# Performance work log

Hardware: AMD Instinct MI355X
Metric: run time of the kernel (lower is better)

The kernel has to match this reference:

```python
import jax, jax.numpy as jnp
import numpy as np

B, L, N = 32, 512, 512          # batch, seq_len, enc_in (num variables = token dim)
D, H, EL, DF = 512, 8, 2, 2048  # d_model, n_heads (hardcoded 8 in FourierBlock), e_layers, d_ff
PRED, K, MODES = 96, 25, 64     # pred_len, moving_avg kernel, fourier modes (low select)
E = D // H


def setup_inputs() -> dict:
    key = jax.random.key(0)
    ks = jax.random.split(key, 16)
    s = 0.02
    return {
        "x_enc": jax.random.normal(ks[0], (B, L, N), jnp.float32),
        "x_mark_enc": jax.random.normal(ks[1], (B, L, 4), jnp.float32),
        "x_dec": jax.random.normal(ks[2], (B, 144, N), jnp.float32),
        "x_mark_dec": jax.random.normal(ks[3], (B, 144, 4), jnp.float32),
        "W_trend": jax.random.normal(ks[4], (L, PRED), jnp.float32) * s,
        "b_trend": jnp.zeros((PRED,), jnp.float32),
        "W_emb": jax.random.normal(ks[5], (L, D), jnp.float32) * s,
        "b_emb": jnp.zeros((D,), jnp.float32),
        "Wq": jax.random.normal(ks[6], (EL, D, D), jnp.float32) * s,
        "bq": jnp.zeros((EL, D), jnp.float32),
        "Wk": jax.random.normal(ks[7], (EL, D, D), jnp.float32) * s,
        "bk": jnp.zeros((EL, D), jnp.float32),
        "Wv": jax.random.normal(ks[8], (EL, D, D), jnp.float32) * s,
        "bv": jnp.zeros((EL, D), jnp.float32),
        "fw_r": jax.random.uniform(ks[9], (EL, H, E, E, MODES), jnp.float32) / (D * D),
        "fw_i": jax.random.uniform(ks[10], (EL, H, E, E, MODES), jnp.float32) / (D * D),
        "Wo": jax.random.normal(ks[11], (EL, D, D), jnp.float32) * s,
        "bo": jnp.zeros((EL, D), jnp.float32),
        "W1": jax.random.normal(ks[12], (EL, DF, D), jnp.float32) * s,
        "W2": jax.random.normal(ks[13], (EL, D, DF), jnp.float32) * s,
        "ln_g": jnp.ones((D,), jnp.float32),
        "ln_b": jnp.zeros((D,), jnp.float32),
        "W_head": jax.random.normal(ks[14], (D, PRED), jnp.float32) * s,
        "b_head": jnp.zeros((PRED,), jnp.float32),
    }


def series_decomp(x, k):
    # moving average over axis=1 with edge replication padding (Autoformer style)
    pad = (k - 1) // 2
    xp = jnp.concatenate([jnp.repeat(x[:, :1], pad, axis=1), x,
                          jnp.repeat(x[:, -1:], pad, axis=1)], axis=1)
    c = jnp.cumsum(xp, axis=1)
    c = jnp.concatenate([jnp.zeros_like(c[:, :1]), c], axis=1)
    mean = (c[:, k:] - c[:, :-k]) / k
    return x - mean, mean


def fourier_attn(x, Wq, bq, Wk, bk, Wv, bv, fw, Wo, bo):
    # AutoCorrelationLayer wrapping FourierBlock (k/v projections computed but unused)
    b, n, d = x.shape
    q = (x @ Wq + bq).reshape(b, n, H, E)
    _k = (x @ Wk + bk).reshape(b, n, H, E)
    _v = (x @ Wv + bv).reshape(b, n, H, E)
    xq = jnp.transpose(q, (0, 2, 3, 1))        # [B,H,E,N]
    x_ft = jnp.fft.rfft(xq, axis=-1)           # [B,H,E,N//2+1]
    m = fw.shape[-1]
    # low-frequency mode select: index = range(m); out_ft[..., wi] = einsum('bhi,hio->bho')
    out_sel = jnp.einsum('bhim,hiom->bhom', x_ft[..., :m], fw)
    out_ft = jnp.zeros((b, H, E, n // 2 + 1), x_ft.dtype).at[..., :m].set(out_sel)
    xt = jnp.fft.irfft(out_ft, n=n, axis=-1)   # [B,H,E,N]
    out = xt.reshape(b, n, H * E)              # replicates torch .view(B, L, -1) on [B,H,E,L]
    return out @ Wo + bo


def encoder_layer(x, Wq, bq, Wk, bk, Wv, bv, fw, Wo, bo, W1, W2):
    x = x + fourier_attn(x, Wq, bq, Wk, bk, Wv, bv, fw, Wo, bo)
    x, _ = series_decomp(x, K)
    y = jax.nn.gelu(x @ W1.T, approximate=False) @ W2.T  # 1x1 convs, bias=False
    x, _ = series_decomp(x + y, K)
    return x


def my_layernorm(x, g, b):
    mu = jnp.mean(x, -1, keepdims=True)
    var = jnp.var(x, -1, keepdims=True)
    xh = (x - mu) / jnp.sqrt(var + 1e-5) * g + b
    return xh - jnp.mean(xh, axis=1, keepdims=True)  # my_Layernorm: subtract seq-mean


def reference(x_enc, x_mark_enc, x_dec, x_mark_dec, W_trend, b_trend, W_emb, b_emb,
              Wq, bq, Wk, bk, Wv, bv, fw_r, fw_i, Wo, bo, W1, W2, ln_g, ln_b,
              W_head, b_head):
    seasonal, trend = series_decomp(x_enc, K)                         # [B,L,N]
    trend_out = jnp.einsum('bln,lp->bpn', trend, W_trend) + b_trend[None, :, None]
    enc = jnp.einsum('bln,ld->bnd', seasonal, W_emb) + b_emb          # variate tokens [B,N,D]
    for i in range(EL):
        fw = fw_r[i] + 1j * fw_i[i]
        enc = encoder_layer(enc, Wq[i], bq[i], Wk[i], bk[i], Wv[i], bv[i],
                            fw, Wo[i], bo[i], W1[i], W2[i])
    enc = my_layernorm(enc, ln_g, ln_b)
    seasonal_out = jnp.transpose(enc @ W_head + b_head, (0, 2, 1))    # [B,pred,N]
    return seasonal_out + trend_out
```

## Files before the change

kernel.cpp:

```cpp
#include <hip/hip_runtime.h>
#include <math.h>


typedef unsigned short ushort_t;
typedef unsigned int uint_t;
using bf16x8_t = __attribute__((ext_vector_type(8))) short;
using f32x4_t  = __attribute__((ext_vector_type(4))) float;
using u16x8_t  = __attribute__((ext_vector_type(8))) unsigned short;

__device__ __forceinline__ unsigned short f2b(float x) {
    union { float f; uint_t u; } c; c.f = x;
    uint_t r = c.u + 0x7fffu + ((c.u >> 16) & 1u);
    return (unsigned short)(r >> 16);
}
__device__ __forceinline__ float b2f(unsigned short h) {
    union { uint_t u; float f; } c; c.u = ((uint_t)h) << 16; return c.f;
}
__device__ __forceinline__ float gelu_exact(float v) {
    return 0.5f * v * (1.0f + erff(v * 0.70710678118654752f));
}

#define GCAST(p) ((const __attribute__((address_space(1))) void*)(p))
#define LCAST(p) ((__attribute__((address_space(3))) void*)(p))

enum { ME_F32 = 0, ME_BF16, ME_DCBIAS_BF16, ME_BIASCOL_BF16,
       ME_BIASCOL_ACCB16, ME_GELU_BF16, ME_RESB_BF16, ME_TREND };

template<int EPI>
__global__ __launch_bounds__(512)
void mgemm_k(const ushort_t* __restrict__ A, const ushort_t* __restrict__ B,
             const float* __restrict__ bias, const ushort_t* __restrict__ Resb,
             void* __restrict__ Cv,
             int M, int N, int K, int ldc, int ldres,
             long sA, long sB, long sC, long sRes)
{
    const int gx = gridDim.x, gy = gridDim.y;
    const int nwg = gx * gy * gridDim.z;
    const int lin = (blockIdx.z * gy + blockIdx.y) * gx + blockIdx.x;
    const int cpx = nwg >> 3;
    const int swz = (nwg & 7) ? lin : ((lin & 7) * cpx + (lin >> 3));
    const int bx = swz % gx;
    const int t2 = swz / gx;
    const int by = t2 % gy;
    const int bz = t2 / gy;

    A += bz * sA;
    B += bz * sB;
    const int m0 = by * 128, n0 = bx * 128;

    __shared__ __align__(16) ushort_t As[3][4096];
    __shared__ __align__(16) ushort_t Bs[3][4096];

    const int tid = threadIdx.x;
    const int wave = tid >> 6, lane = tid & 63;
    const int wr = wave >> 1, wc = wave & 1;

    f32x4_t acc[2][4] = {};

    const int srow = tid >> 2;
    const int skof = (tid & 3) * 8;

    const ushort_t* ga = A + (long)(m0 + srow) * K + skof;
    const ushort_t* gb = B + (long)(n0 + srow) * K + skof;
    const int nt = K >> 5;

#define STG(s, bidx) { const long ko = (long)(s) << 5; \
    __builtin_amdgcn_global_load_lds(GCAST(ga + ko), LCAST(As[bidx] + wave * 512), 16, 0, 0); \
    __builtin_amdgcn_global_load_lds(GCAST(gb + ko), LCAST(Bs[bidx] + wave * 512), 16, 0, 0); }

    STG(0, 0)
    STG(1, 1)

    const int kg = (lane >> 4) * 8;
    int cb = 0;

    for (int t = 0; t < nt; ++t) {
        if (t + 1 < nt) { asm volatile("s_waitcnt vmcnt(2)" ::: "memory"); }
        else            { asm volatile("s_waitcnt vmcnt(0)" ::: "memory"); }
        __builtin_amdgcn_s_barrier();
        asm volatile("" ::: "memory");
        __builtin_amdgcn_sched_barrier(0);
        if (t + 2 < nt) { int nb = cb + 2; if (nb >= 3) nb -= 3; STG(t + 2, nb) }

        bf16x8_t a[2], b[4];
        #pragma unroll
        for (int i = 0; i < 2; ++i)
            a[i] = *(const bf16x8_t*)&As[cb][(wr * 32 + i * 16 + (lane & 15)) * 32 + kg];
        #pragma unroll
        for (int j = 0; j < 4; ++j)
            b[j] = *(const bf16x8_t*)&Bs[cb][(wc * 64 + j * 16 + (lane & 15)) * 32 + kg];
        #pragma unroll
        for (int i = 0; i < 2; ++i)
            #pragma unroll
            for (int j = 0; j < 4; ++j)
                acc[i][j] = __builtin_amdgcn_mfma_f32_16x16x32_bf16(a[i], b[j], acc[i][j], 0, 0, 0);
        ++cb; if (cb >= 3) cb = 0;
    }
#undef STG

    float*    Cf  = (float*)Cv + bz * sC;
    ushort_t* Cb  = (ushort_t*)Cv + bz * sC;
    const ushort_t* R = Resb ? Resb + bz * sRes : nullptr;

    #pragma unroll
    for (int i = 0; i < 2; ++i) {
        #pragma unroll
        for (int j = 0; j < 4; ++j) {
            #pragma unroll
            for (int r = 0; r < 4; ++r) {
                int gm = m0 + wr * 32 + i * 16 + (lane >> 4) * 4 + r;
                int gn = n0 + wc * 64 + j * 16 + (lane & 15);
                float v = acc[i][j][r];
                long idx = (long)gm * ldc + gn;
                if (EPI == ME_F32)               Cf[idx] = v;
                else if (EPI == ME_BF16)         Cb[idx] = f2b(v);
                else if (EPI == ME_DCBIAS_BF16)  Cb[idx] = f2b(v + (gn == 0 ? 512.f * bias[gm] : 0.f));
                else if (EPI == ME_BIASCOL_BF16) Cb[idx] = f2b(v + bias[gn]);
                else if (EPI == ME_BIASCOL_ACCB16) Cb[idx] = f2b(b2f(Cb[idx]) + v + bias[gn]);
                else if (EPI == ME_GELU_BF16)    Cb[idx] = f2b(gelu_exact(v));
                else if (EPI == ME_RESB_BF16)    Cb[idx] = f2b(v + b2f(R[(long)gm * ldres + gn]));
                else if (EPI == ME_TREND) { if (gm < 96) Cf[idx] = v + bias[gm]; }
            }
        }
    }
}

__global__ __launch_bounds__(256)
void fmix_k(const ushort_t* __restrict__ A2, const ushort_t* __restrict__ B2,
            ushort_t* __restrict__ OS)
{
    const int hm = blockIdx.x;
    const int h = hm >> 6, m = hm & 63;
    __shared__ __align__(16) ushort_t As[32 * 128];
    __shared__ __align__(16) ushort_t Bs[128 * 128];

    const int tid = threadIdx.x;
    const int w = tid >> 6, lane = tid & 63;

    const ushort_t* Ag = A2 + (long)hm * 4096;
    const ushort_t* Bg = B2 + (long)hm * 16384;
    #pragma unroll
    for (int r = 0; r < 2; ++r)
        __builtin_amdgcn_global_load_lds(GCAST(Ag + w * 1024 + r * 512 + lane * 8),
                                         LCAST(As + w * 1024 + r * 512), 16, 0, 0);
    #pragma unroll
    for (int r = 0; r < 8; ++r)
        __builtin_amdgcn_global_load_lds(GCAST(Bg + w * 4096 + r * 512 + lane * 8),
                                         LCAST(Bs + w * 4096 + r * 512), 16, 0, 0);
    __syncthreads();

    f32x4_t acc[2][2] = {};
    const int kg = (lane >> 4) * 8;
    #pragma unroll
    for (int kk = 0; kk < 4; ++kk) {
        bf16x8_t a[2], b[2];
        #pragma unroll
        for (int i = 0; i < 2; ++i)
            a[i] = *(const bf16x8_t*)&As[(i * 16 + (lane & 15)) * 128 + kk * 32 + kg];
        #pragma unroll
        for (int j = 0; j < 2; ++j)
            b[j] = *(const bf16x8_t*)&Bs[(w * 32 + j * 16 + (lane & 15)) * 128 + kk * 32 + kg];
        #pragma unroll
        for (int i = 0; i < 2; ++i)
            #pragma unroll
            for (int j = 0; j < 2; ++j)
                acc[i][j] = __builtin_amdgcn_mfma_f32_16x16x32_bf16(a[i], b[j], acc[i][j], 0, 0, 0);
    }

    #pragma unroll
    for (int i = 0; i < 2; ++i) {
        #pragma unroll
        for (int j = 0; j < 2; ++j) {
            #pragma unroll
            for (int r = 0; r < 4; ++r) {
                int b = i * 16 + (lane >> 4) * 4 + r;
                int n2 = w * 32 + j * 16 + (lane & 15);
                int o = n2 & 63, ri = n2 >> 6;
                OS[((long)b * 512 + h * 64 + o) * 128 + ri * 64 + m] = f2b(acc[i][j][r]);
            }
        }
    }
}

__global__ __launch_bounds__(256)
void bprep_k(const float* __restrict__ FR, const float* __restrict__ FI,
             ushort_t* __restrict__ B2)
{
    const int bx = blockIdx.x;
    const int h = bx >> 6, o = bx & 63;
    __shared__ float fr_s[64][65];
    __shared__ float fi_s[64][65];
    for (int e = threadIdx.x; e < 4096; e += 256) {
        int i = e >> 6, m = e & 63;
        long src = ((long)(h * 64 + i) * 64 + o) * 64 + m;
        fr_s[i][m] = FR[src];
        fi_s[i][m] = FI[src];
    }
    __syncthreads();
    const int m = threadIdx.x & 63;
    const int kq = threadIdx.x >> 6;
    ushort_t* b0 = B2 + ((long)(h * 64 + m) * 128 + o) * 128;
    ushort_t* b1 = B2 + ((long)(h * 64 + m) * 128 + o + 64) * 128;
    for (int kk = 0; kk < 32; ++kk) {
        int k2 = kq * 32 + kk;
        int ik = k2 & 63, hi = k2 >> 6;
        float fr = fr_s[ik][m], fi = fi_s[ik][m];
        b0[k2] = f2b(hi ? -fi : fr);
        b1[k2] = f2b(hi ?  fr : fi);
    }
}

__global__ __launch_bounds__(256)
void aprep_k(const ushort_t* __restrict__ XFTb, ushort_t* __restrict__ A2)
{
    const int bx = blockIdx.x;
    const int b = bx >> 3, h = bx & 7;
    __shared__ ushort_t xs[64][130];
    for (int e = threadIdx.x; e < 8192; e += 256) {
        int i = e >> 7, mp = e & 127;
        xs[i][mp] = XFTb[((long)b * 512 + h * 64 + i) * 128 + mp];
    }
    __syncthreads();
    const int m = threadIdx.x & 63;
    const int kq = threadIdx.x >> 6;
    ushort_t* dst = A2 + ((long)(h * 64 + m) * 32 + b) * 128;
    for (int kk = 0; kk < 32; ++kk) {
        int k2 = kq * 32 + kk;
        int i = k2 & 63, ri = k2 >> 6;
        dst[k2] = xs[i][ri * 64 + m];
    }
}

__global__ __launch_bounds__(256)
void decomp2_k(const float* __restrict__ X, ushort_t* __restrict__ Sb,
               ushort_t* __restrict__ Trb)
{
    const int id = blockIdx.x;
    const int ch = id & 1, rc = (id >> 1) & 31, b = id >> 6;
    const int c = ch * 256 + threadIdx.x;
    const int r0 = rc * 16;
    const long base = ((long)b << 18) + c;
    float s = 0.f;
    #pragma unroll
    for (int j = -12; j <= 12; ++j) {
        int rr = r0 + j; rr = rr < 0 ? 0 : (rr > 511 ? 511 : rr);
        s += X[base + ((long)rr << 9)];
    }
    for (int rr = 0; rr < 16; ++rr) {
        int r = r0 + rr;
        float mean = s * (1.f / 25.f);
        long idx = base + ((long)r << 9);
        float x = X[idx];
        if (Sb)  Sb[idx] = f2b(x - mean);
        if (Trb) Trb[idx] = f2b(mean);
        int rp = r + 13; rp = rp > 511 ? 511 : rp;
        int rm = r - 12; rm = rm < 0 ? 0 : rm;
        s += X[base + ((long)rp << 9)] - X[base + ((long)rm << 9)];
    }
}

__global__ __launch_bounds__(256)
void decomp2h_k(const ushort_t* __restrict__ Xb, ushort_t* __restrict__ Sb)
{
    const int id = blockIdx.x;
    const int ch = id & 1, rc = (id >> 1) & 31, b = id >> 6;
    const int c = ch * 256 + threadIdx.x;
    const int r0 = rc * 16;
    const long base = ((long)b << 18) + c;
    float s = 0.f;
    #pragma unroll
    for (int j = -12; j <= 12; ++j) {
        int rr = r0 + j; rr = rr < 0 ? 0 : (rr > 511 ? 511 : rr);
        s += b2f(Xb[base + ((long)rr << 9)]);
    }
    for (int rr = 0; rr < 16; ++rr) {
        int r = r0 + rr;
        float mean = s * (1.f / 25.f);
        long idx = base + ((long)r << 9);
        float x = b2f(Xb[idx]);
        Sb[idx] = f2b(x - mean);
        int rp = r + 13; rp = rp > 511 ? 511 : rp;
        int rm = r - 12; rm = rm < 0 ? 0 : rm;
        s += b2f(Xb[base + ((long)rp << 9)]) - b2f(Xb[base + ((long)rm << 9)]);
    }
}

__global__ __launch_bounds__(256)
void init_tables_k(ushort_t* __restrict__ TFb, ushort_t* __restrict__ TI2b)
{
    int t = blockIdx.x * 256 + threadIdx.x;
    const float w = 6.283185307179586f / 512.f;
    if (t < 65536) {
        int mp = t >> 9, n = t & 511;
        int m = mp & 63;
        float ang = ((m * n) & 511) * w;
        TFb[t] = f2b((mp < 64) ? cosf(ang) : -sinf(ang));
    } else {
        int u = t - 65536;
        int mp = u >> 9, n = u & 511;
        int m = mp & 63;
        float ang = ((m * n) & 511) * w;
        float v;
        if (mp < 64) v = (m == 0) ? (1.f / 512.f) : (2.f / 512.f) * cosf(ang);
        else         v = (m == 0) ? 0.f : -(2.f / 512.f) * sinf(ang);
        TI2b[u] = f2b(v);
    }
}

__global__ __launch_bounds__(256)
void f2b_k(const float* __restrict__ X, ushort_t* __restrict__ Y, long n)
{
    long i = ((long)blockIdx.x * 256 + threadIdx.x) * 8;
    if (i >= n) return;
    const float4* xp = (const float4*)(X + i);
    float4 v0 = xp[0], v1 = xp[1];
    u16x8_t o;
    o[0] = f2b(v0.x); o[1] = f2b(v0.y); o[2] = f2b(v0.z); o[3] = f2b(v0.w);
    o[4] = f2b(v1.x); o[5] = f2b(v1.y); o[6] = f2b(v1.z); o[7] = f2b(v1.w);
    *(u16x8_t*)(Y + i) = o;
}

__global__ __launch_bounds__(256)
void trans_b_k(const float* __restrict__ X, ushort_t* __restrict__ Y,
               int R, int C, long sX, long sY)
{
    __shared__ float t[32][33];
    X += (long)blockIdx.z * sX;
    Y += (long)blockIdx.z * sY;
    int r0 = blockIdx.y * 32, c0 = blockIdx.x * 32;
    int tx = threadIdx.x & 31, ty = threadIdx.x >> 5;
    #pragma unroll
    for (int i = ty; i < 32; i += 8)
        t[i][tx] = X[(long)(r0 + i) * C + c0 + tx];
    __syncthreads();
    #pragma unroll
    for (int i = ty; i < 32; i += 8)
        Y[(long)(c0 + i) * R + r0 + tx] = f2b(t[tx][i]);
}

__global__ __launch_bounds__(256)
void trans_bb_k(const ushort_t* __restrict__ X, ushort_t* __restrict__ Y,
                int R, int C, long sX, long sY)
{
    __shared__ ushort_t t[32][34];
    X += (long)blockIdx.z * sX;
    Y += (long)blockIdx.z * sY;
    int r0 = blockIdx.y * 32, c0 = blockIdx.x * 32;
    int tx = threadIdx.x & 31, ty = threadIdx.x >> 5;
    #pragma unroll
    for (int i = ty; i < 32; i += 8)
        t[i][tx] = X[(long)(r0 + i) * C + c0 + tx];
    __syncthreads();
    #pragma unroll
    for (int i = ty; i < 32; i += 8)
        Y[(long)(c0 + i) * R + r0 + tx] = t[tx][i];
}

__global__ __launch_bounds__(256)
void ln_rows_bb_k(const ushort_t* __restrict__ Xb, const float* __restrict__ g,
                  const float* __restrict__ bta, ushort_t* __restrict__ Yb)
{
    int wave = threadIdx.x >> 6, lane = threadIdx.x & 63;
    long row = (long)blockIdx.x * 4 + wave;
    const ushort_t* x = Xb + row * 512 + lane * 8;
    u16x8_t v = *(const u16x8_t*)x;
    float f[8];
    float s = 0.f, ss = 0.f;
    #pragma unroll
    for (int j = 0; j < 8; ++j) { f[j] = b2f(v[j]); s += f[j]; ss += f[j] * f[j]; }
    #pragma unroll
    for (int o = 32; o; o >>= 1) { s += __shfl_xor(s, o); ss += __shfl_xor(ss, o); }
    float mu = s * (1.f / 512.f);
    float var = ss * (1.f / 512.f) - mu * mu;
    float inv = rsqrtf(var + 1e-5f);
    u16x8_t ov;
    #pragma unroll
    for (int j = 0; j < 8; ++j)
        ov[j] = f2b((f[j] - mu) * inv * g[lane * 8 + j] + bta[lane * 8 + j]);
    *(u16x8_t*)(Yb + row * 512 + lane * 8) = ov;
}

__global__ __launch_bounds__(256)
void colmean_bb_k(const ushort_t* __restrict__ Y, ushort_t* __restrict__ O)
{
    __shared__ float ps[4][64];
    int b = blockIdx.x, dg = blockIdx.y;
    int wave = threadIdx.x >> 6, lane = threadIdx.x & 63;
    int d = dg * 64 + lane;
    long base = (long)b * 262144 + d;
    float s = 0.f;
    for (int t = wave * 128; t < wave * 128 + 128; ++t)
        s += b2f(Y[base + ((long)t << 9)]);
    ps[wave][lane] = s;
    __syncthreads();
    float mean = (ps[0][lane] + ps[1][lane] + ps[2][lane] + ps[3][lane]) * (1.f / 512.f);
    for (int t = wave * 128; t < wave * 128 + 128; ++t)
        O[base + ((long)t << 9)] = f2b(b2f(Y[base + ((long)t << 9)]) - mean);
}

__global__ __launch_bounds__(256)
void headadd_k(const float* __restrict__ Th, const float* __restrict__ bh,
               float* __restrict__ out)
{
    const int id = blockIdx.x;
    const int b = id >> 4, t0 = (id & 15) * 32;
    __shared__ float tile[32][100];
    for (int e = threadIdx.x; e < 32 * 96; e += 256) {
        int tl = e / 96, p = e - tl * 96;
        tile[tl][p] = Th[((long)(b * 512 + t0 + tl)) * 128 + p];
    }
    __syncthreads();
    for (int e = threadIdx.x; e < 96 * 32; e += 256) {
        int p = e >> 5, tl = e & 31;
        out[(long)b * 49152 + p * 512 + t0 + tl] += tile[tl][p] + bh[p];
    }
}

extern "C" void kernel_launch(void* const* d_in, const int* in_sizes, int n_in,
                              void* d_out, int out_size, void* d_ws, size_t ws_size,
                              hipStream_t stream)
{
    const float* x_enc   = (const float*)d_in[0];
    const float* W_trend = (const float*)d_in[4];
    const float* b_trend = (const float*)d_in[5];
    const float* W_emb   = (const float*)d_in[6];
    const float* b_emb   = (const float*)d_in[7];
    const float* Wq      = (const float*)d_in[8];
    const float* bq      = (const float*)d_in[9];
    const float* fw_r    = (const float*)d_in[14];
    const float* fw_i    = (const float*)d_in[15];
    const float* Wo      = (const float*)d_in[16];
    const float* bo      = (const float*)d_in[17];
    const float* W1      = (const float*)d_in[18];
    const float* W2      = (const float*)d_in[19];
    const float* ln_g    = (const float*)d_in[20];
    const float* ln_b    = (const float*)d_in[21];
    const float* W_head  = (const float*)d_in[22];
    const float* b_head  = (const float*)d_in[23];
    float* out = (float*)d_out;
    float* ws  = (float*)d_ws;

    const long F = 8388608;
    float* G    = ws;
    ushort_t* xw  = (ushort_t*)(ws + 3 * F);
    ushort_t* xs  = (ushort_t*)(ws + 4 * F);
    ushort_t* T1b = xs + 8388608;
    ushort_t* qT  = (ushort_t*)(ws + 5 * F);

    ushort_t* trendb = (ushort_t*)G;
    ushort_t* seasb  = (ushort_t*)(G + 4194304);
    ushort_t* XFTb  = (ushort_t*)G;
    ushort_t* Yb    = (ushort_t*)(G + 1048576);
    ushort_t* A2    = (ushort_t*)(G + 2097152);
    ushort_t* OSELb = (ushort_t*)(G + 3145728);
    ushort_t* xbT   = (ushort_t*)(G + 4194304);
    ushort_t* B2    = (ushort_t*)(G + 8388608);
    float*    Thead = G;
    ushort_t* gb    = (ushort_t*)G;

    ushort_t* WembT  = (ushort_t*)(ws + 6 * F);
    ushort_t* WTq    = WembT + 262144;
    ushort_t* WTo    = WTq + 262144;
    ushort_t* W1b    = WTo + 262144;
    ushort_t* W2b    = W1b + 1048576;
    ushort_t* TFb    = W2b + 1048576;
    ushort_t* TI2b   = TFb + 65536;
    ushort_t* WtT    = TI2b + 65536;
    ushort_t* WheadT = WtT + 65536;
    ushort_t* TIWob  = WheadT + 65536;

    dim3 blk(256), blk5(512);

    init_tables_k<<<dim3(512), blk, 0, stream>>>(TFb, TI2b);

    decomp2_k<<<dim3(2048), blk, 0, stream>>>(x_enc, seasb, trendb);

    trans_b_k<<<dim3(3, 16, 1), blk, 0, stream>>>(W_trend, WtT, 512, 96, 0L, 0L);
    trans_b_k<<<dim3(3, 16, 1), blk, 0, stream>>>(W_head, WheadT, 512, 96, 0L, 0L);
    trans_b_k<<<dim3(16, 16, 1), blk, 0, stream>>>(W_emb, WembT, 512, 512, 0L, 0L);

    trans_bb_k<<<dim3(16, 16, 32), blk, 0, stream>>>(trendb, qT, 512, 512, 262144L, 262144L);
    mgemm_k<ME_TREND><<<dim3(4, 1, 32), blk5, 0, stream>>>(
        WtT, qT, b_trend, nullptr, out,
        128, 512, 512, 512, 0, 0L, 262144L, 49152L, 0L);

    trans_bb_k<<<dim3(16, 16, 32), blk, 0, stream>>>(seasb, qT, 512, 512, 262144L, 262144L);
    mgemm_k<ME_BIASCOL_BF16><<<dim3(4, 4, 32), blk5, 0, stream>>>(
        qT, WembT, b_emb, nullptr, xw,
        512, 512, 512, 512, 0, 262144L, 0L, 262144L, 0L);

    for (int l = 0; l < 2; ++l) {
        const float* Wq_l = Wq + (long)l * 262144;
        const float* bq_l = bq + (long)l * 512;
        const float* Wo_l = Wo + (long)l * 262144;
        const float* bo_l = bo + (long)l * 512;
        const float* W1_l = W1 + (long)l * 1048576;
        const float* W2_l = W2 + (long)l * 1048576;
        const float* fr_l = fw_r + (long)l * 2097152;
        const float* fi_l = fw_i + (long)l * 2097152;

        trans_b_k<<<dim3(16, 16, 1), blk, 0, stream>>>(Wq_l, WTq, 512, 512, 0L, 0L);
        trans_b_k<<<dim3(16, 16, 1), blk, 0, stream>>>(Wo_l, WTo, 512, 512, 0L, 0L);
        f2b_k<<<dim3(512), blk, 0, stream>>>(W1_l, W1b, 1048576L);
        f2b_k<<<dim3(512), blk, 0, stream>>>(W2_l, W2b, 1048576L);
        bprep_k<<<dim3(512), blk, 0, stream>>>(fr_l, fi_l, B2);

        mgemm_k<ME_BF16><<<dim3(1, 4, 1), blk5, 0, stream>>>(
            WTo, TI2b, nullptr, nullptr, TIWob,
            512, 128, 512, 128, 0, 0L, 0L, 0L, 0L);

        trans_bb_k<<<dim3(16, 16, 32), blk, 0, stream>>>(xw, xbT, 512, 512, 262144L, 262144L);

        mgemm_k<ME_BF16><<<dim3(4, 1, 32), blk5, 0, stream>>>(
            TFb, xbT, nullptr, nullptr, Yb,
            128, 512, 512, 512, 0, 0L, 262144L, 65536L, 0L);

        mgemm_k<ME_DCBIAS_BF16><<<dim3(1, 4, 32), blk5, 0, stream>>>(
            WTq, Yb, bq_l, nullptr, XFTb,
            512, 128, 512, 128, 0, 0L, 65536L, 65536L, 0L);

        aprep_k<<<dim3(256), blk, 0, stream>>>(XFTb, A2);
        fmix_k<<<dim3(512), blk, 0, stream>>>(A2, B2, OSELb);

        mgemm_k<ME_BIASCOL_ACCB16><<<dim3(4, 128, 1), blk5, 0, stream>>>(
            OSELb, TIWob, bo_l, nullptr, xw,
            16384, 512, 128, 512, 0, 0L, 0L, 0L, 0L);

        decomp2h_k<<<dim3(2048), blk, 0, stream>>>(xw, xs);

        mgemm_k<ME_GELU_BF16><<<dim3(16, 128, 1), blk5, 0, stream>>>(
            xs, W1b, nullptr, nullptr, gb,
            16384, 2048, 512, 2048, 0, 0L, 0L, 0L, 0L);
        mgemm_k<ME_RESB_BF16><<<dim3(4, 128, 1), blk5, 0, stream>>>(
            gb, W2b, nullptr, xs, T1b,
            16384, 512, 2048, 512, 512, 0L, 0L, 0L, 0L);

        decomp2h_k<<<dim3(2048), blk, 0, stream>>>(T1b, xw);
    }

    ln_rows_bb_k<<<dim3(4096), blk, 0, stream>>>(xw, ln_g, ln_b, T1b);
    colmean_bb_k<<<dim3(32, 8), blk, 0, stream>>>(T1b, xs);

    mgemm_k<ME_F32><<<dim3(1, 128, 1), blk5, 0, stream>>>(
        xs, WheadT, nullptr, nullptr, Thead,
        16384, 128, 512, 128, 0, 0L, 0L, 0L, 0L);

    headadd_k<<<dim3(512), blk, 0, stream>>>(Thead, b_head, out);
}
```

Baseline: 603.1 us.

## Add small-tile GEMM, vectorize decomposition, hoist weight prep, use fast GELU

Adds a 64x64-tile, 256-thread GEMM variant for the small-M/N GEMMs (trend, Fourier projections, head) so they launch more workgroups and fill the GPU better. The series-decomp kernel now handles 8 bf16 columns per thread with vector loads and stores. Weight conversions for both layers are hoisted out of the layer loop into batched launches. Exact erf GELU is replaced by a tanh-style sigmoid approximation, which lowers epilogue cost but changes numerics.

Result: faster. 564.9 us (-6.3%).

```diff
diff --git a/kernel.cpp b/kernel.cpp
--- a/kernel.cpp
+++ b/kernel.cpp
@@ -16,8 +16,9 @@
 __device__ __forceinline__ float b2f(unsigned short h) {
     union { uint_t u; float f; } c; c.u = ((uint_t)h) << 16; return c.f;
 }
-__device__ __forceinline__ float gelu_exact(float v) {
-    return 0.5f * v * (1.0f + erff(v * 0.70710678118654752f));
+__device__ __forceinline__ float gelu_fast(float x) {
+    float z = x * (1.5957691216f + 0.0713548163f * x * x);
+    return x / (1.f + __expf(-z));
 }
 
 #define GCAST(p) ((const __attribute__((address_space(1))) void*)(p))
@@ -114,11 +115,102 @@
                 long idx = (long)gm * ldc + gn;
                 if (EPI == ME_F32)               Cf[idx] = v;
                 else if (EPI == ME_BF16)         Cb[idx] = f2b(v);
-                else if (EPI == ME_DCBIAS_BF16)  Cb[idx] = f2b(v + (gn == 0 ? 512.f * bias[gm] : 0.f));
                 else if (EPI == ME_BIASCOL_BF16) Cb[idx] = f2b(v + bias[gn]);
                 else if (EPI == ME_BIASCOL_ACCB16) Cb[idx] = f2b(b2f(Cb[idx]) + v + bias[gn]);
-                else if (EPI == ME_GELU_BF16)    Cb[idx] = f2b(gelu_exact(v));
+                else if (EPI == ME_GELU_BF16)    Cb[idx] = f2b(gelu_fast(v));
                 else if (EPI == ME_RESB_BF16)    Cb[idx] = f2b(v + b2f(R[(long)gm * ldres + gn]));
+            }
+        }
+    }
+}
+
+template<int EPI>
+__global__ __launch_bounds__(256)
+void sgemm_k(const ushort_t* __restrict__ A, const ushort_t* __restrict__ B,
+             const float* __restrict__ bias, void* __restrict__ Cv,
+             int M, int N, int K, int ldc,
+             long sA, long sB, long sC)
+{
+    const int gx = gridDim.x, gy = gridDim.y;
+    const int nwg = gx * gy * gridDim.z;
+    const int lin = (blockIdx.z * gy + blockIdx.y) * gx + blockIdx.x;
+    const int cpx = nwg >> 3;
+    const int swz = (nwg & 7) ? lin : ((lin & 7) * cpx + (lin >> 3));
+    const int bx = swz % gx;
+    const int t2 = swz / gx;
+    const int by = t2 % gy;
+    const int bz = t2 / gy;
+
+    A += bz * sA;
+    B += bz * sB;
+    const int m0 = by * 64, n0 = bx * 64;
+
+    __shared__ __align__(16) ushort_t As[3][2048];
+    __shared__ __align__(16) ushort_t Bs[3][2048];
+
+    const int tid = threadIdx.x;
+    const int wave = tid >> 6, lane = tid & 63;
+    const int wr = wave >> 1, wc = wave & 1;
+
+    f32x4_t acc[2][2] = {};
+
+    const int srow = tid >> 2;
+    const int skof = (tid & 3) * 8;
+
+    const ushort_t* ga = A + (long)(m0 + srow) * K + skof;
+    const ushort_t* gb = B + (long)(n0 + srow) * K + skof;
+    const int nt = K >> 5;
+
+#define STG(s, bidx) { const long ko = (long)(s) << 5; \
+    __builtin_amdgcn_global_load_lds(GCAST(ga + ko), LCAST(As[bidx] + wave * 512), 16, 0, 0); \
+    __builtin_amdgcn_global_load_lds(GCAST(gb + ko), LCAST(Bs[bidx] + wave * 512), 16, 0, 0); }
+
+    STG(0, 0)
+    STG(1, 1)
+
+    const int kg = (lane >> 4) * 8;
+    int cb = 0;
+
+    for (int t = 0; t < nt; ++t) {
+        if (t + 1 < nt) { asm volatile("s_waitcnt vmcnt(2)" ::: "memory"); }
+        else            { asm volatile("s_waitcnt vmcnt(0)" ::: "memory"); }
+        __builtin_amdgcn_s_barrier();
+        asm volatile("" ::: "memory");
+        __builtin_amdgcn_sched_barrier(0);
+        if (t + 2 < nt) { int nb = cb + 2; if (nb >= 3) nb -= 3; STG(t + 2, nb) }
+
+        bf16x8_t a[2], b[2];
+        #pragma unroll
+        for (int i = 0; i < 2; ++i)
+            a[i] = *(const bf16x8_t*)&As[cb][(wr * 32 + i * 16 + (lane & 15)) * 32 + kg];
+        #pragma unroll
+        for (int j = 0; j < 2; ++j)
+            b[j] = *(const bf16x8_t*)&Bs[cb][(wc * 32 + j * 16 + (lane & 15)) * 32 + kg];
+        #pragma unroll
+        for (int i = 0; i < 2; ++i)
+            #pragma unroll
+            for (int j = 0; j < 2; ++j)
+                acc[i][j] = __builtin_amdgcn_mfma_f32_16x16x32_bf16(a[i], b[j], acc[i][j], 0, 0, 0);
+        ++cb; if (cb >= 3) cb = 0;
+    }
+#undef STG
+
+    float*    Cf = (float*)Cv + bz * sC;
+    ushort_t* Cb = (ushort_t*)Cv + bz * sC;
+
+    #pragma unroll
+    for (int i = 0; i < 2; ++i) {
+        #pragma unroll
+        for (int j = 0; j < 2; ++j) {
+            #pragma unroll
+            for (int r = 0; r < 4; ++r) {
+                int gm = m0 + wr * 32 + i * 16 + (lane >> 4) * 4 + r;
+                int gn = n0 + wc * 32 + j * 16 + (lane & 15);
+                float v = acc[i][j][r];
+                long idx = (long)gm * ldc + gn;
+                if (EPI == ME_F32)               Cf[idx] = v;
+                else if (EPI == ME_BF16)         Cb[idx] = f2b(v);
+                else if (EPI == ME_DCBIAS_BF16)  Cb[idx] = f2b(v + (gn == 0 ? 512.f * bias[gm] : 0.f));
                 else if (EPI == ME_TREND) { if (gm < 96) Cf[idx] = v + bias[gm]; }
             }
         }
@@ -260,28 +352,37 @@
 }
 
 __global__ __launch_bounds__(256)
-void decomp2h_k(const ushort_t* __restrict__ Xb, ushort_t* __restrict__ Sb)
+void decomp2v_k(const ushort_t* __restrict__ Xb, ushort_t* __restrict__ Sb)
 {
     const int id = blockIdx.x;
-    const int ch = id & 1, rc = (id >> 1) & 31, b = id >> 6;
-    const int c = ch * 256 + threadIdx.x;
-    const int r0 = rc * 16;
-    const long base = ((long)b << 18) + c;
-    float s = 0.f;
+    const int b = id >> 4, rc = id & 15;
+    const int c0 = (threadIdx.x & 63) * 8;
+    const int rsub = threadIdx.x >> 6;
+    const int r0 = rc * 32 + rsub * 8;
+    const ushort_t* base = Xb + ((long)b << 18) + c0;
+    ushort_t* obase = Sb + ((long)b << 18) + c0;
+
+    float s[8] = {};
     #pragma unroll
     for (int j = -12; j <= 12; ++j) {
         int rr = r0 + j; rr = rr < 0 ? 0 : (rr > 511 ? 511 : rr);
-        s += b2f(Xb[base + ((long)rr << 9)]);
-    }
-    for (int rr = 0; rr < 16; ++rr) {
+        u16x8_t v = *(const u16x8_t*)(base + ((long)rr << 9));
+        #pragma unroll
+        for (int k = 0; k < 8; ++k) s[k] += b2f(v[k]);
+    }
+    for (int rr = 0; rr < 8; ++rr) {
         int r = r0 + rr;
-        float mean = s * (1.f / 25.f);
-        long idx = base + ((long)r << 9);
-        float x = b2f(Xb[idx]);
-        Sb[idx] = f2b(x - mean);
+        u16x8_t xv = *(const u16x8_t*)(base + ((long)r << 9));
+        u16x8_t ov;
+        #pragma unroll
+        for (int k = 0; k < 8; ++k) ov[k] = f2b(b2f(xv[k]) - s[k] * (1.f / 25.f));
+        *(u16x8_t*)(obase + ((long)r << 9)) = ov;
         int rp = r + 13; rp = rp > 511 ? 511 : rp;
         int rm = r - 12; rm = rm < 0 ? 0 : rm;
-        s += b2f(Xb[base + ((long)rp << 9)]) - b2f(Xb[base + ((long)rm << 9)]);
+        u16x8_t vp = *(const u16x8_t*)(base + ((long)rp << 9));
+        u16x8_t vm = *(const u16x8_t*)(base + ((long)rm << 9));
+        #pragma unroll
+        for (int k = 0; k < 8; ++k) s[k] += b2f(vp[k]) - b2f(vm[k]);
     }
 }
 
@@ -459,15 +560,15 @@
     ushort_t* gb    = (ushort_t*)G;
 
     ushort_t* WembT  = (ushort_t*)(ws + 6 * F);
-    ushort_t* WTq    = WembT + 262144;
-    ushort_t* WTo    = WTq + 262144;
-    ushort_t* W1b    = WTo + 262144;
-    ushort_t* W2b    = W1b + 1048576;
-    ushort_t* TFb    = W2b + 1048576;
+    ushort_t* WTq2   = WembT + 262144;
+    ushort_t* WTo2   = WTq2 + 524288;
+    ushort_t* W1b2   = WTo2 + 524288;
+    ushort_t* W2b2   = W1b2 + 2097152;
+    ushort_t* TFb    = W2b2 + 2097152;
     ushort_t* TI2b   = TFb + 65536;
     ushort_t* WtT    = TI2b + 65536;
     ushort_t* WheadT = WtT + 65536;
-    ushort_t* TIWob  = WheadT + 65536;
+    ushort_t* TIWob2 = WheadT + 65536;
 
     dim3 blk(256), blk5(512);
 
@@ -478,11 +579,18 @@
     trans_b_k<<<dim3(3, 16, 1), blk, 0, stream>>>(W_trend, WtT, 512, 96, 0L, 0L);
     trans_b_k<<<dim3(3, 16, 1), blk, 0, stream>>>(W_head, WheadT, 512, 96, 0L, 0L);
     trans_b_k<<<dim3(16, 16, 1), blk, 0, stream>>>(W_emb, WembT, 512, 512, 0L, 0L);
+    trans_b_k<<<dim3(16, 16, 2), blk, 0, stream>>>(Wq, WTq2, 512, 512, 262144L, 262144L);
+    trans_b_k<<<dim3(16, 16, 2), blk, 0, stream>>>(Wo, WTo2, 512, 512, 262144L, 262144L);
+    f2b_k<<<dim3(1024), blk, 0, stream>>>(W1, W1b2, 2097152L);
+    f2b_k<<<dim3(1024), blk, 0, stream>>>(W2, W2b2, 2097152L);
+    sgemm_k<ME_BF16><<<dim3(2, 8, 2), blk, 0, stream>>>(
+        WTo2, TI2b, nullptr, TIWob2,
+        512, 128, 512, 128, 262144L, 0L, 65536L);
 
     trans_bb_k<<<dim3(16, 16, 32), blk, 0, stream>>>(trendb, qT, 512, 512, 262144L, 262144L);
-    mgemm_k<ME_TREND><<<dim3(4, 1, 32), blk5, 0, stream>>>(
-        WtT, qT, b_trend, nullptr, out,
-        128, 512, 512, 512, 0, 0L, 262144L, 49152L, 0L);
+    sgemm_k<ME_TREND><<<dim3(8, 2, 32), blk, 0, stream>>>(
+        WtT, qT, b_trend, out,
+        128, 512, 512, 512, 0L, 262144L, 49152L);
 
     trans_bb_k<<<dim3(16, 16, 32), blk, 0, stream>>>(seasb, qT, 512, 512, 262144L, 262144L);
     mgemm_k<ME_BIASCOL_BF16><<<dim3(4, 4, 32), blk5, 0, stream>>>(
@@ -490,60 +598,52 @@
         512, 512, 512, 512, 0, 262144L, 0L, 262144L, 0L);
 
     for (int l = 0; l < 2; ++l) {
-        const float* Wq_l = Wq + (long)l * 262144;
         const float* bq_l = bq + (long)l * 512;
-        const float* Wo_l = Wo + (long)l * 262144;
         const float* bo_l = bo + (long)l * 512;
-        const float* W1_l = W1 + (long)l * 1048576;
-        const float* W2_l = W2 + (long)l * 1048576;
         const float* fr_l = fw_r + (long)l * 2097152;
         const float* fi_l = fw_i + (long)l * 2097152;
-
-        trans_b_k<<<dim3(16, 16, 1), blk, 0, stream>>>(Wq_l, WTq, 512, 512, 0L, 0L);
-        trans_b_k<<<dim3(16, 16, 1), blk, 0, stream>>>(Wo_l, WTo, 512, 512, 0L, 0L);
-        f2b_k<<<dim3(512), blk, 0, stream>>>(W1_l, W1b, 1048576L);
-        f2b_k<<<dim3(512), blk, 0, stream>>>(W2_l, W2b, 1048576L);
+        const ushort_t* WTq_l   = WTq2 + (long)l * 262144;
+        const ushort_t* W1b_l   = W1b2 + (long)l * 1048576;
+        const ushort_t* W2b_l   = W2b2 + (long)l * 1048576;
+        const ushort_t* TIWob_l = TIWob2 + (long)l * 65536;
+
         bprep_k<<<dim3(512), blk, 0, stream>>>(fr_l, fi_l, B2);
 
-        mgemm_k<ME_BF16><<<dim3(1, 4, 1), blk5, 0, stream>>>(
-            WTo, TI2b, nullptr, nullptr, TIWob,
-            512, 128, 512, 128, 0, 0L, 0L, 0L, 0L);
-
         trans_bb_k<<<dim3(16, 16, 32), blk, 0, stream>>>(xw, xbT, 512, 512, 262144L, 262144L);
 
-        mgemm_k<ME_BF16><<<dim3(4, 1, 32), blk5, 0, stream>>>(
-            TFb, xbT, nullptr, nullptr, Yb,
-            128, 512, 512, 512, 0, 0L, 262144L, 65536L, 0L);
-
-        mgemm_k<ME_DCBIAS_BF16><<<dim3(1, 4, 32), blk5, 0, stream>>>(
-            WTq, Yb, bq_l, nullptr, XFTb,
-            512, 128, 512, 128, 0, 0L, 65536L, 65536L, 0L);
+        sgemm_k<ME_BF16><<<dim3(8, 2, 32), blk, 0, stream>>>(
+            TFb, xbT, nullptr, Yb,
+            128, 512, 512, 512, 0L, 262144L, 65536L);
+
+        sgemm_k<ME_DCBIAS_BF16><<<dim3(2, 8, 32), blk, 0, stream>>>(
+            WTq_l, Yb, bq_l, XFTb,
+            512, 128, 512, 128, 0L, 65536L, 65536L);
 
         aprep_k<<<dim3(256), blk, 0, stream>>>(XFTb, A2);
         fmix_k<<<dim3(512), blk, 0, stream>>>(A2, B2, OSELb);
 
         mgemm_k<ME_BIASCOL_ACCB16><<<dim3(4, 128, 1), blk5, 0, stream>>>(
-            OSELb, TIWob, bo_l, nullptr, xw,
+            OSELb, TIWob_l, bo_l, nullptr, xw,
             16384, 512, 128, 512, 0, 0L, 0L, 0L, 0L);
 
-        decomp2h_k<<<dim3(2048), blk, 0, stream>>>(xw, xs);
+        decomp2v_k<<<dim3(512), blk, 0, stream>>>(xw, xs);
 
         mgemm_k<ME_GELU_BF16><<<dim3(16, 128, 1), blk5, 0, stream>>>(
-            xs, W1b, nullptr, nullptr, gb,
+            xs, W1b_l, nullptr, nullptr, gb,
             16384, 2048, 512, 2048, 0, 0L, 0L, 0L, 0L);
         mgemm_k<ME_RESB_BF16><<<dim3(4, 128, 1), blk5, 0, stream>>>(
-            gb, W2b, nullptr, xs, T1b,
+            gb, W2b_l, nullptr, xs, T1b,
             16384, 512, 2048, 512, 512, 0L, 0L, 0L, 0L);
 
-        decomp2h_k<<<dim3(2048), blk, 0, stream>>>(T1b, xw);
+        decomp2v_k<<<dim3(512), blk, 0, stream>>>(T1b, xw);
     }
 
     ln_rows_bb_k<<<dim3(4096), blk, 0, stream>>>(xw, ln_g, ln_b, T1b);
     colmean_bb_k<<<dim3(32, 8), blk, 0, stream>>>(T1b, xs);
 
-    mgemm_k<ME_F32><<<dim3(1, 128, 1), blk5, 0, stream>>>(
-        xs, WheadT, nullptr, nullptr, Thead,
-        16384, 128, 512, 128, 0, 0L, 0L, 0L, 0L);
+    sgemm_k<ME_F32><<<dim3(2, 256, 1), blk, 0, stream>>>(
+        xs, WheadT, nullptr, Thead,
+        16384, 128, 512, 128, 0L, 0L, 0L);
 
     headadd_k<<<dim3(512), blk, 0, stream>>>(Thead, b_head, out);
 }
```
